# Optimization experiments

Measured on AMD Instinct MI355X. Metric: run time of the kernel, lower is better.

Reference implementation:

```python
import jax, jax.numpy as jnp
import numpy as np

B, S, D, H, K = 2, 2048, 1024, 16, 64


def setup_inputs() -> dict:
    key = jax.random.key(0)
    k1, k2, k3 = jax.random.split(key, 3)
    x = jax.random.normal(k1, (B, S, D), dtype=jnp.float32)
    # causal mask: 1 where query can attend to key (key_pos <= pos)
    mask = jnp.tril(jnp.ones((S, S), dtype=jnp.float32))
    W_qkv = jax.random.normal(k2, (D, 3, H, K), dtype=jnp.float32) * 0.02
    b_qkv = jnp.zeros((3, H, K), dtype=jnp.float32)
    W_proj = jax.random.normal(k3, (H, K, D), dtype=jnp.float32) * 0.02
    b_proj = jnp.zeros((D,), dtype=jnp.float32)
    return {"x": x, "mask": mask, "W_qkv": W_qkv, "b_qkv": b_qkv,
            "W_proj": W_proj, "b_proj": b_proj, "layer_idx": 0}


def reference(x, mask, W_qkv, b_qkv, W_proj, b_proj, layer_idx):
    # c_attn: [B,S,D] @ [D,3,H,K] -> [B,S,3,H,K]
    qkv = jnp.einsum('bsd,dthk->bsthk', x, W_qkv) + b_qkv
    q, k, v = qkv[:, :, 0], qkv[:, :, 1], qkv[:, :, 2]  # each [B,S,H,K]
    scale = jax.lax.rsqrt(float(K))  # scale_attn_by_inverse_layer_idx=False
    q = q * scale
    # attn scores over key_size: [B,H,S(pos),S(key_pos)]
    scores = jnp.einsum('bshk,bthk->bhst', q, k)
    scores = scores + (1.0 - mask) * -1e9
    weights = jax.nn.softmax(scores, axis=-1).astype(x.dtype)
    # attn_pdrop = 0.0 -> dropout is identity
    attn_out = jnp.einsum('bhst,bthk->bshk', weights, v)  # [B,S,H,K]
    out = jnp.einsum('bshk,hkd->bsd', attn_out, W_proj) + b_proj
    return out
```

## Files before the change

### kernel.cpp

```cpp
#include <hip/hip_runtime.h>

typedef __bf16 bf16x8 __attribute__((ext_vector_type(8)));
typedef float f32x4 __attribute__((ext_vector_type(4)));
typedef float f32x16 __attribute__((ext_vector_type(16)));
typedef unsigned short u16x8 __attribute__((ext_vector_type(8)));

constexpr int S_LEN = 2048;
constexpr int QKV1  = 2 * 16 * 2048 * 64;

__device__ inline unsigned short f2bf(float f) {
    __bf16 h = (__bf16)f;
    return __builtin_bit_cast(unsigned short, h);
}

__device__ inline void gll16(const void* g, void* l) {
    __builtin_amdgcn_global_load_lds(
        (const __attribute__((address_space(1))) unsigned int*)g,
        (__attribute__((address_space(3))) unsigned int*)l,
        16, 0, 0);
}

__global__ __launch_bounds__(256) void cvt_f32_bf16(
    const float* __restrict__ src, unsigned short* __restrict__ dst, int n4)
{
    int i = blockIdx.x * 256 + threadIdx.x;
    if (i >= n4) return;
    float4 v = ((const float4*)src)[i];
    ushort4 u;
    u.x = f2bf(v.x); u.y = f2bf(v.y); u.z = f2bf(v.z); u.w = f2bf(v.w);
    ((ushort4*)dst)[i] = u;
}

__global__ __launch_bounds__(256) void transpose_cvt(
    const float* __restrict__ src, unsigned short* __restrict__ dst, int R, int C)
{
    __shared__ float t[32][33];
    const int c0 = blockIdx.x * 32, r0 = blockIdx.y * 32;
    const int tx = threadIdx.x, ty = threadIdx.y;
    #pragma unroll
    for (int i = 0; i < 4; ++i)
        t[ty * 4 + i][tx] = src[(size_t)(r0 + ty * 4 + i) * C + c0 + tx];
    __syncthreads();
    #pragma unroll
    for (int i = 0; i < 4; ++i)
        dst[(size_t)(c0 + ty * 4 + i) * R + r0 + tx] = f2bf(t[tx][ty * 4 + i]);
}

template<int EPI>
__global__ __launch_bounds__(256) void gemm128(
    const unsigned short* __restrict__ A,
    const unsigned short* __restrict__ Bt,
    const float* __restrict__ bias,
    void* __restrict__ outp, int M, int N, int K)
{
    __shared__ unsigned short As[2][128 * 32];
    __shared__ unsigned short Bs[2][128 * 32];
    const int tid = threadIdx.x, lane = tid & 63, wid = tid >> 6;
    const int q = lane & 15, g = lane >> 4;
    const int wr = wid >> 1, wc = wid & 1;

    const int nbx = N >> 7;
    const int cpx = gridDim.x >> 3;
    const int bid = blockIdx.x;
    const int swz = (bid & 7) * cpx + (bid >> 3);
    const int m0 = (swz / nbx) * 128, n0 = (swz % nbx) * 128;

    const int srow_in = lane >> 2;
    const int sslot   = (lane & 3) ^ (srow_in & 3);
    auto stage = [&](int buf, int k0) {
        #pragma unroll
        for (int i = 0; i < 2; ++i) {
            int c = wid * 2 + i;
            int row = c * 16 + srow_in;
            gll16(&A [(size_t)(m0 + row) * K + k0 + sslot * 8], &As[buf][c * 512]);
            gll16(&Bt[(size_t)(n0 + row) * K + k0 + sslot * 8], &Bs[buf][c * 512]);
        }
    };

    f32x4 acc[4][4];
    #pragma unroll
    for (int i = 0; i < 4; ++i)
        #pragma unroll
        for (int j = 0; j < 4; ++j) acc[i][j] = (f32x4){0.f, 0.f, 0.f, 0.f};

    const int NSTEP = K >> 5;
    const int rslot = (g ^ (q & 3)) * 8;
    stage(0, 0);
    __syncthreads();
    int cur = 0;

    for (int ks = 0; ks < NSTEP; ++ks) {
        if (ks + 1 < NSTEP) stage(cur ^ 1, (ks + 1) * 32);
        bf16x8 a[4], b[4];
        #pragma unroll
        for (int mi = 0; mi < 4; ++mi)
            a[mi] = *(const bf16x8*)&As[cur][(wr * 64 + mi * 16 + q) * 32 + rslot];
        #pragma unroll
        for (int ni = 0; ni < 4; ++ni)
            b[ni] = *(const bf16x8*)&Bs[cur][(wc * 64 + ni * 16 + q) * 32 + rslot];
        #pragma unroll
        for (int mi = 0; mi < 4; ++mi)
            #pragma unroll
            for (int ni = 0; ni < 4; ++ni)
                acc[mi][ni] = __builtin_amdgcn_mfma_f32_16x16x32_bf16(a[mi], b[ni], acc[mi][ni], 0, 0, 0);
        __syncthreads();
        cur ^= 1;
    }

    #pragma unroll
    for (int mi = 0; mi < 4; ++mi)
        #pragma unroll
        for (int ni = 0; ni < 4; ++ni)
            #pragma unroll
            for (int r = 0; r < 4; ++r) {
                int m = m0 + wr * 64 + mi * 16 + g * 4 + r;
                int n = n0 + wc * 64 + ni * 16 + q;
                float v = acc[mi][ni][r] + bias[n];
                if (EPI == 0) {
                    int t = n >> 10, rem = n & 1023;
                    if (t == 0) v *= 0.125f;
                    int h2 = rem >> 6, kk = rem & 63;
                    int bb = m >> 11, s = m & 2047;
                    size_t off;
                    if (t == 2)
                        off = 2 * (size_t)QKV1 + ((size_t)(bb * 16 + h2) * 64 + kk) * 2048 + s;
                    else
                        off = (size_t)t * QKV1 + ((size_t)(bb * 16 + h2) * 2048 + s) * 64 + kk;
                    ((unsigned short*)outp)[off] = f2bf(v);
                } else {
                    ((float*)outp)[(size_t)m * N + n] = v;
                }
            }
}

__global__ __launch_bounds__(256) void attn_fwd(
    const unsigned short* __restrict__ qkv, unsigned short* __restrict__ aout)
{
    __shared__ unsigned short Ks[2][64][72];
    __shared__ unsigned short Vs[2][64][72];
    __shared__ float cLds[4][32];
    const int tid = threadIdx.x, lane = tid & 63, wid = tid >> 6;
    const int hi = lane >> 5, lq = lane & 31;
    const int bh = blockIdx.x;
    const int t  = 15 - (int)blockIdx.y;
    const int NJ = 2 * t + 2;
    const unsigned short* Qg = qkv + (size_t)bh * S_LEN * 64;
    const unsigned short* Kg = qkv + (size_t)QKV1 + (size_t)bh * S_LEN * 64;
    const unsigned short* Vt = qkv + 2 * (size_t)QKV1 + (size_t)bh * 64 * S_LEN;

    const int srr = tid >> 3, scc = (tid & 7) * 8;
    u16x8 kr[2], vr[2];
    auto stage_load = [&](int j0) {
        #pragma unroll
        for (int p = 0; p < 2; ++p) {
            kr[p] = *(const u16x8*)&Kg[(size_t)(j0 + srr + p * 32) * 64 + scc];
            vr[p] = *(const u16x8*)&Vt[(size_t)(srr + p * 32) * 2048 + j0 + scc];
        }
    };
    auto stage_write = [&](int b) {
        #pragma unroll
        for (int p = 0; p < 2; ++p) {
            *(u16x8*)&Ks[b][srr + p * 32][scc] = kr[p];
            *(u16x8*)&Vs[b][srr + p * 32][scc] = vr[p];
        }
    };

    const int bb = bh >> 4, h = bh & 15;
    const int qbase = t * 128 + wid * 32;
    const int qg = qbase + lq;

    bf16x8 qf[4];
    #pragma unroll
    for (int kc = 0; kc < 4; ++kc)
        qf[kc] = *(const bf16x8*)&Qg[(size_t)qg * 64 + kc * 16 + hi * 8];

    f32x16 z16;
    #pragma unroll
    for (int j = 0; j < 16; ++j) z16[j] = 0.f;

    f32x16 o0 = z16, o1 = z16;
    float m = -1e30f, lr = 0.f;

    stage_load(0);
    stage_write(0);
    int cur = 0;

    for (int jb = 0; jb < NJ; ++jb) {
        const int j0 = jb * 64;
        if (jb + 1 < NJ) stage_load(j0 + 64);
        __syncthreads();

        if (j0 <= qbase + 31) {
            f32x16 s0, s1;
            __builtin_amdgcn_s_setprio(1);
            {
                bf16x8 k0 = *(const bf16x8*)&Ks[cur][lq][hi * 8];
                bf16x8 k1 = *(const bf16x8*)&Ks[cur][32 + lq][hi * 8];
                s0 = __builtin_amdgcn_mfma_f32_32x32x16_bf16(k0, qf[0], z16, 0, 0, 0);
                s1 = __builtin_amdgcn_mfma_f32_32x32x16_bf16(k1, qf[0], z16, 0, 0, 0);
            }
            #pragma unroll
            for (int kc = 1; kc < 4; ++kc) {
                bf16x8 k0 = *(const bf16x8*)&Ks[cur][lq][kc * 16 + hi * 8];
                bf16x8 k1 = *(const bf16x8*)&Ks[cur][32 + lq][kc * 16 + hi * 8];
                s0 = __builtin_amdgcn_mfma_f32_32x32x16_bf16(k0, qf[kc], s0, 0, 0, 0);
                s1 = __builtin_amdgcn_mfma_f32_32x32x16_bf16(k1, qf[kc], s1, 0, 0, 0);
            }
            __builtin_amdgcn_s_setprio(0);
            if (j0 + 63 > qbase) {
                #pragma unroll
                for (int r = 0; r < 16; ++r) {
                    int kv0 = j0 + (r & 3) + 8 * (r >> 2) + 4 * hi;
                    if (kv0 > qg)      s0[r] = -1e30f;
                    if (kv0 + 32 > qg) s1[r] = -1e30f;
                }
            }
            float tm[8];
            #pragma unroll
            for (int j = 0; j < 8; ++j)
                tm[j] = fmaxf(fmaxf(s0[j], s0[j + 8]), fmaxf(s1[j], s1[j + 8]));
            float pm_loc = fmaxf(fmaxf(fmaxf(tm[0], tm[1]), fmaxf(tm[2], tm[3])),
                                 fmaxf(fmaxf(tm[4], tm[5]), fmaxf(tm[6], tm[7])));
            if (!__all(pm_loc <= m + 8.0f)) {
                float pm = fmaxf(pm_loc, __shfl_xor(pm_loc, 32));
                float mn = fmaxf(m, pm);
                float corr = __expf(m - mn);
                m = mn; lr *= corr;
                if (lane < 32) cLds[wid][lq] = corr;
                #pragma unroll
                for (int r = 0; r < 16; ++r) {
                    float cq = cLds[wid][(r & 3) + 8 * (r >> 2) + 4 * hi];
                    o0[r] *= cq; o1[r] *= cq;
                }
            }
            float p0[16], p1[16], ts[16];
            #pragma unroll
            for (int j = 0; j < 16; ++j) {
                p0[j] = __expf(s0[j] - m);
                p1[j] = __expf(s1[j] - m);
                ts[j] = p0[j] + p1[j];
            }
            #pragma unroll
            for (int w = 8; w > 0; w >>= 1)
                #pragma unroll
                for (int j = 0; j < w; ++j) ts[j] += ts[j + w];
            lr += ts[0];
            int w0[8], w1[8];
            #pragma unroll
            for (int j = 0; j < 8; ++j) {
                asm("v_cvt_pk_bf16_f32 %0, %1, %2" : "=v"(w0[j]) : "v"(p0[2 * j]), "v"(p0[2 * j + 1]));
                asm("v_cvt_pk_bf16_f32 %0, %1, %2" : "=v"(w1[j]) : "v"(p1[2 * j]), "v"(p1[2 * j + 1]));
            }
            bf16x8 pa[4];
            auto mkfrag = [&](const int* w, int base) -> bf16x8 {
                int x0 = __shfl_xor(w[base + 0], 32);
                int x1 = __shfl_xor(w[base + 1], 32);
                int x2 = __shfl_xor(w[base + 2], 32);
                int x3 = __shfl_xor(w[base + 3], 32);
                int4 f;
                f.x = hi ? x2          : w[base + 0];
                f.y = hi ? x3          : w[base + 1];
                f.z = hi ? w[base + 2] : x0;
                f.w = hi ? w[base + 3] : x1;
                return __builtin_bit_cast(bf16x8, f);
            };
            pa[0] = mkfrag(w0, 0);
            pa[1] = mkfrag(w0, 4);
            pa[2] = mkfrag(w1, 0);
            pa[3] = mkfrag(w1, 4);
            __builtin_amdgcn_s_setprio(1);
            #pragma unroll
            for (int kc = 0; kc < 4; ++kc) {
                bf16x8 v0 = *(const bf16x8*)&Vs[cur][lq][kc * 16 + hi * 8];
                bf16x8 v1 = *(const bf16x8*)&Vs[cur][32 + lq][kc * 16 + hi * 8];
                o0 = __builtin_amdgcn_mfma_f32_32x32x16_bf16(pa[kc], v0, o0, 0, 0, 0);
                o1 = __builtin_amdgcn_mfma_f32_32x32x16_bf16(pa[kc], v1, o1, 0, 0, 0);
            }
            __builtin_amdgcn_s_setprio(0);
        }

        if (jb + 1 < NJ) stage_write(cur ^ 1);
        cur ^= 1;
    }

    float lr_full = lr + __shfl_xor(lr, 32);
    float inv = 1.0f / lr_full;
    if (lane < 32) cLds[wid][lq] = inv;
    #pragma unroll
    for (int r = 0; r < 16; ++r) {
        float iq = cLds[wid][(r & 3) + 8 * (r >> 2) + 4 * hi];
        int srow_g = qbase + (r & 3) + 8 * (r >> 2) + 4 * hi;
        size_t rowoff = (size_t)(bb * 2048 + srow_g) * 1024 + h * 64;
        aout[rowoff + lq]      = f2bf(o0[r] * iq);
        aout[rowoff + 32 + lq] = f2bf(o1[r] * iq);
    }
}

extern "C" void kernel_launch(void* const* d_in, const int* in_sizes, int n_in,
                              void* d_out, int out_size, void* d_ws, size_t ws_size,
                              hipStream_t stream) {
    const float* x     = (const float*)d_in[0];
    const float* Wqkv  = (const float*)d_in[2];
    const float* bqkv  = (const float*)d_in[3];
    const float* Wproj = (const float*)d_in[4];
    const float* bproj = (const float*)d_in[5];

    unsigned short* qkvb  = (unsigned short*)d_ws;
    unsigned short* aoutb = qkvb + 3 * (size_t)QKV1;
    unsigned short* Wt   = aoutb;
    unsigned short* Wt2  = qkvb;
    unsigned short* Xbf  = (unsigned short*)d_out;

    cvt_f32_bf16<<<4096, 256, 0, stream>>>(x, Xbf, 4096 * 1024 / 4);
    transpose_cvt<<<dim3(96, 32), dim3(32, 8), 0, stream>>>(Wqkv, Wt, 1024, 3072);
    gemm128<0><<<768, 256, 0, stream>>>(Xbf, Wt, bqkv, qkvb, 4096, 3072, 1024);
    attn_fwd<<<dim3(32, 16), 256, 0, stream>>>(qkvb, aoutb);
    transpose_cvt<<<dim3(32, 32), dim3(32, 8), 0, stream>>>(Wproj, Wt2, 1024, 1024);
    gemm128<1><<<256, 256, 0, stream>>>(aoutb, Wt2, bproj, d_out, 4096, 1024, 1024);
}
```

Before: 131.4 us.

## Split attention KV range across two blocks and merge partials in combine kernel

Each causal query tile's key range is split in half across two workgroups, which doubles the grid and evens out the load between long and short tiles. Partial unnormalized outputs are written in bf16 along with each row's running max and sum, and a new combine kernel rescales and merges the two halves into the final attention output. The aim is better occupancy and less tail imbalance, at the cost of an extra launch, extra memory traffic for the partials, and some precision loss from storing the partials in bf16. The partials reuse the output buffer as scratch.

```diff
diff --git a/kernel.cpp b/kernel.cpp
--- a/kernel.cpp
+++ b/kernel.cpp
@@ -134,7 +134,8 @@
 }
 
 __global__ __launch_bounds__(256) void attn_fwd(
-    const unsigned short* __restrict__ qkv, unsigned short* __restrict__ aout)
+    const unsigned short* __restrict__ qkv,
+    unsigned short* __restrict__ po, float2* __restrict__ pml)
 {
     __shared__ unsigned short Ks[2][64][72];
     __shared__ unsigned short Vs[2][64][72];
@@ -142,8 +143,11 @@
     const int tid = threadIdx.x, lane = tid & 63, wid = tid >> 6;
     const int hi = lane >> 5, lq = lane & 31;
     const int bh = blockIdx.x;
-    const int t  = 15 - (int)blockIdx.y;
-    const int NJ = 2 * t + 2;
+    const int uy = (int)blockIdx.y;
+    const int t    = 15 - (uy >> 1);
+    const int half = uy & 1;
+    const int jb0 = half ? (t + 1) : 0;
+    const int jb1 = half ? (2 * t + 2) : (t + 1);
     const unsigned short* Qg = qkv + (size_t)bh * S_LEN * 64;
     const unsigned short* Kg = qkv + (size_t)QKV1 + (size_t)bh * S_LEN * 64;
     const unsigned short* Vt = qkv + 2 * (size_t)QKV1 + (size_t)bh * 64 * S_LEN;
@@ -165,7 +169,6 @@
         }
     };
 
-    const int bb = bh >> 4, h = bh & 15;
     const int qbase = t * 128 + wid * 32;
     const int qg = qbase + lq;
 
@@ -181,13 +184,13 @@
     f32x16 o0 = z16, o1 = z16;
     float m = -1e30f, lr = 0.f;
 
-    stage_load(0);
+    stage_load(jb0 * 64);
     stage_write(0);
     int cur = 0;
 
-    for (int jb = 0; jb < NJ; ++jb) {
+    for (int jb = jb0; jb < jb1; ++jb) {
         const int j0 = jb * 64;
-        if (jb + 1 < NJ) stage_load(j0 + 64);
+        if (jb + 1 < jb1) stage_load(j0 + 64);
         __syncthreads();
 
         if (j0 <= qbase + 31) {
@@ -279,20 +282,57 @@
             __builtin_amdgcn_s_setprio(0);
         }
 
-        if (jb + 1 < NJ) stage_write(cur ^ 1);
+        if (jb + 1 < jb1) stage_write(cur ^ 1);
         cur ^= 1;
     }
 
+    const int unit = (bh * 16 + t) * 2 + half;
     float lr_full = lr + __shfl_xor(lr, 32);
-    float inv = 1.0f / lr_full;
-    if (lane < 32) cLds[wid][lq] = inv;
+    if (lane < 32) {
+        float2 v; v.x = m; v.y = lr_full;
+        pml[unit * 128 + wid * 32 + lq] = v;
+    }
     #pragma unroll
     for (int r = 0; r < 16; ++r) {
-        float iq = cLds[wid][(r & 3) + 8 * (r >> 2) + 4 * hi];
-        int srow_g = qbase + (r & 3) + 8 * (r >> 2) + 4 * hi;
-        size_t rowoff = (size_t)(bb * 2048 + srow_g) * 1024 + h * 64;
-        aout[rowoff + lq]      = f2bf(o0[r] * iq);
-        aout[rowoff + 32 + lq] = f2bf(o1[r] * iq);
+        int lrow = wid * 32 + (r & 3) + 8 * (r >> 2) + 4 * hi;
+        size_t off = ((size_t)unit * 128 + lrow) * 64;
+        po[off + lq]      = f2bf(o0[r]);
+        po[off + 32 + lq] = f2bf(o1[r]);
+    }
+}
+
+__global__ __launch_bounds__(256) void attn_combine(
+    const unsigned short* __restrict__ po, const float2* __restrict__ pml,
+    unsigned short* __restrict__ aout)
+{
+    const int gid = blockIdx.x * 256 + threadIdx.x;
+    const int row = gid >> 2;
+    const int cg  = (gid & 3) * 16;
+    const int bt = row >> 7, lrow = row & 127;
+    const float2 ml0 = pml[(bt * 2 + 0) * 128 + lrow];
+    const float2 ml1 = pml[(bt * 2 + 1) * 128 + lrow];
+    const float ms = fmaxf(ml0.x, ml1.x);
+    float w0 = __expf(ml0.x - ms), w1 = __expf(ml1.x - ms);
+    const float inv = 1.0f / (ml0.y * w0 + ml1.y * w1);
+    w0 *= inv; w1 *= inv;
+    const size_t r0 = ((size_t)(bt * 2 + 0) * 128 + lrow) * 64 + cg;
+    const size_t r1 = ((size_t)(bt * 2 + 1) * 128 + lrow) * 64 + cg;
+    const int bh = bt >> 4, t = bt & 15;
+    const int bb = bh >> 4, h = bh & 15;
+    const int s = t * 128 + lrow;
+    const size_t orow = ((size_t)(bb * 2048 + s)) * 1024 + h * 64 + cg;
+    #pragma unroll
+    for (int c = 0; c < 2; ++c) {
+        u16x8 a = *(const u16x8*)&po[r0 + c * 8];
+        u16x8 b = *(const u16x8*)&po[r1 + c * 8];
+        u16x8 o;
+        #pragma unroll
+        for (int e = 0; e < 8; ++e) {
+            float fa = __builtin_bit_cast(float, (unsigned)((unsigned short)a[e]) << 16);
+            float fb = __builtin_bit_cast(float, (unsigned)((unsigned short)b[e]) << 16);
+            o[e] = f2bf(fa * w0 + fb * w1);
+        }
+        *(u16x8*)&aout[orow + c * 8] = o;
     }
 }
 
@@ -307,14 +347,17 @@
 
     unsigned short* qkvb  = (unsigned short*)d_ws;
     unsigned short* aoutb = qkvb + 3 * (size_t)QKV1;
+    float2*         pml   = (float2*)(aoutb + 4096 * 1024);
     unsigned short* Wt   = aoutb;
     unsigned short* Wt2  = qkvb;
     unsigned short* Xbf  = (unsigned short*)d_out;
+    unsigned short* po   = (unsigned short*)d_out;
 
     cvt_f32_bf16<<<4096, 256, 0, stream>>>(x, Xbf, 4096 * 1024 / 4);
     transpose_cvt<<<dim3(96, 32), dim3(32, 8), 0, stream>>>(Wqkv, Wt, 1024, 3072);
     gemm128<0><<<768, 256, 0, stream>>>(Xbf, Wt, bqkv, qkvb, 4096, 3072, 1024);
-    attn_fwd<<<dim3(32, 16), 256, 0, stream>>>(qkvb, aoutb);
+    attn_fwd<<<dim3(32, 32), 256, 0, stream>>>(qkvb, po, pml);
+    attn_combine<<<1024, 256, 0, stream>>>(po, pml, aoutb);
     transpose_cvt<<<dim3(32, 32), dim3(32, 8), 0, stream>>>(Wproj, Wt2, 1024, 1024);
     gemm128<1><<<256, 256, 0, stream>>>(aoutb, Wt2, bproj, d_out, 4096, 1024, 1024);
 }
```

Result: faster. 123.6 us (-6.0%).
